# Kernel tuning notes

Hardware: AMD Instinct MI355X
Metric: run time of the kernel (lower is better)

## Reference

```python
import jax, jax.numpy as jnp
import numpy as np

N_NODES = 50000
N_EDGES = 400000
D_IN = 256
D_OUT = 256
DROPOUT_P = 0.1


def setup_inputs() -> dict:
    key = jax.random.key(0)
    k_feat, k_w, k_src, k_dst = jax.random.split(key, 4)
    feat = jax.random.normal(k_feat, (N_NODES, D_IN), dtype=jnp.float32)
    # Glorot-ish init for the GraphConv weight
    W = jax.random.normal(k_w, (D_IN, D_OUT), dtype=jnp.float32) * (1.0 / np.sqrt(D_IN))
    b = jnp.zeros((D_OUT,), dtype=jnp.float32)
    src = jax.random.randint(k_src, (N_EDGES,), 0, N_NODES, dtype=jnp.int32)
    dst = jax.random.randint(k_dst, (N_EDGES,), 0, N_NODES, dtype=jnp.int32)
    return {"feat": feat, "W": W, "b": b, "src": src, "dst": dst}


def reference(feat, W, b, src, dst):
    # Degrees from the edge list (DGL GraphConv norm='both'):
    # src is normalized by out-degree, dst by in-degree; clamp to >= 1.
    ones = jnp.ones((src.shape[0],), dtype=feat.dtype)
    deg_out = jnp.clip(jax.ops.segment_sum(ones, src, num_segments=N_NODES), 1.0)
    deg_in = jnp.clip(jax.ops.segment_sum(ones, dst, num_segments=N_NODES), 1.0)

    # Pre-normalize, project, then gather-scatter aggregate (mult W first,
    # mathematically identical to DGL's ordering since dims are equal).
    x = feat * jax.lax.rsqrt(deg_out)[:, None]          # [N, D_in]
    x = x @ W                                            # [N, D_out]
    agg = jax.ops.segment_sum(x[src], dst, num_segments=N_NODES)  # [N, D_out]
    h = agg * jax.lax.rsqrt(deg_in)[:, None] + b

    # Activation + dropout (training-mode, deterministic key)
    h = jax.nn.relu(h)
    keep = jax.random.bernoulli(jax.random.key(42), 1.0 - DROPOUT_P, h.shape)
    h = jnp.where(keep, h / (1.0 - DROPOUT_P), 0.0)
    return h
```

## Files before the change

### kernel.cpp

```cpp
#include <hip/hip_runtime.h>
#include <stdint.h>

#define N_NODES 50000
#define N_EDGES 400000
#define DDIM 256
#define MASK_WORDS 400000
#define EDGE_CAP 64
#define EDGE_BLOCKS 782
#define MASK_BLOCKS 1563
#define FCONV_BLOCKS 6250

typedef __attribute__((ext_vector_type(8))) short bf16x8;
typedef __attribute__((ext_vector_type(4))) float f32x4;

__device__ __forceinline__ uint32_t rotl32(uint32_t x, uint32_t r) {
  return (x << r) | (x >> (32u - r));
}

__device__ __forceinline__ uint32_t threefry_draw_0_42(uint32_t x0, uint32_t x1) {
  const uint32_t k0 = 0u, k1 = 42u;
  const uint32_t k2 = k0 ^ k1 ^ 0x1BD11BDAu;
  x0 += k0;
  x1 += k1;
#define TF_ROUND(r)          \
  {                          \
    x0 += x1;                \
    x1 = rotl32(x1, r);      \
    x1 ^= x0;                \
  }
  TF_ROUND(13) TF_ROUND(15) TF_ROUND(26) TF_ROUND(6)
  x0 += k1; x1 += k2 + 1u;
  TF_ROUND(17) TF_ROUND(29) TF_ROUND(16) TF_ROUND(24)
  x0 += k2; x1 += k0 + 2u;
  TF_ROUND(13) TF_ROUND(15) TF_ROUND(26) TF_ROUND(6)
  x0 += k0; x1 += k1 + 3u;
  TF_ROUND(17) TF_ROUND(29) TF_ROUND(16) TF_ROUND(24)
  x0 += k1; x1 += k2 + 4u;
  TF_ROUND(13) TF_ROUND(15) TF_ROUND(26) TF_ROUND(6)
  x0 += k2; x1 += k0 + 5u;
#undef TF_ROUND
  return x0 ^ x1;
}

__device__ __forceinline__ uint16_t bf16_rne(float x) {
  uint32_t u = __float_as_uint(x);
  u += 0x7FFFu + ((u >> 16) & 1u);
  return (uint16_t)(u >> 16);
}

__global__ __launch_bounds__(256) void setup_kernel(
    const float* __restrict__ W, uint16_t* __restrict__ Wt,
    int4* __restrict__ zero_base) {
  const int bid = blockIdx.x;
  if (bid < 98) {
    const int t = bid * 256 + threadIdx.x;
    if (t < 25000) zero_base[t] = make_int4(0, 0, 0, 0);
  } else {
    const int t = (bid - 98) * 256 + threadIdx.x;
    const int n = t >> 6;
    const int k4 = (t & 63) << 2;
    ushort4 p;
    p.x = bf16_rne(W[(size_t)(k4 + 0) * DDIM + n]);
    p.y = bf16_rne(W[(size_t)(k4 + 1) * DDIM + n]);
    p.z = bf16_rne(W[(size_t)(k4 + 2) * DDIM + n]);
    p.w = bf16_rne(W[(size_t)(k4 + 3) * DDIM + n]);
    *(ushort4*)(Wt + (size_t)n * DDIM + k4) = p;
  }
}

__global__ __launch_bounds__(256) void mega_prep_kernel(
    const float* __restrict__ feat, const int* __restrict__ src,
    const int* __restrict__ dst, int* __restrict__ deg_out,
    int* __restrict__ deg_in, int* __restrict__ esrc,
    uint32_t* __restrict__ mask, uint16_t* __restrict__ featb) {
  const int bid = blockIdx.x;
  if (bid < EDGE_BLOCKS) {
    const int base = (bid * 256 + threadIdx.x) * 2;
    if (base < N_EDGES) {
      const int2 s2 = *(const int2*)(src + base);
      const int2 d2 = *(const int2*)(dst + base);
      atomicAdd(&deg_out[s2.x], 1);
      atomicAdd(&deg_out[s2.y], 1);
      const int p0 = atomicAdd(&deg_in[d2.x], 1);
      const int p1 = atomicAdd(&deg_in[d2.y], 1);
      if (p0 < EDGE_CAP) esrc[(d2.x << 6) + p0] = s2.x;
      if (p1 < EDGE_CAP) esrc[(d2.y << 6) + p1] = s2.y;
    }
  } else if (bid < EDGE_BLOCKS + MASK_BLOCKS) {
    const uint32_t t =
        (uint32_t)(bid - EDGE_BLOCKS) * 256u + (uint32_t)threadIdx.x;
    if (t < MASK_WORDS) {
      const uint32_t base = t * 32u;
      uint32_t w = 0u;
#pragma unroll
      for (uint32_t b = 0; b < 32u; ++b) {
        const uint32_t bits = threefry_draw_0_42(0u, base + b);
        w |= ((bits >> 9) < 7549747u) ? (1u << b) : 0u;
      }
      mask[t] = w;
    }
  } else {
    const int t = (bid - EDGE_BLOCKS - MASK_BLOCKS) * 256 + threadIdx.x;
    const size_t base = (size_t)t * 8;
    const float4 a = *(const float4*)(feat + base);
    const float4 b = *(const float4*)(feat + base + 4);
    ushort4 lo, hi;
    lo.x = bf16_rne(a.x); lo.y = bf16_rne(a.y);
    lo.z = bf16_rne(a.z); lo.w = bf16_rne(a.w);
    hi.x = bf16_rne(b.x); hi.y = bf16_rne(b.y);
    hi.z = bf16_rne(b.z); hi.w = bf16_rne(b.w);
    *(ushort4*)(featb + base) = lo;
    *(ushort4*)(featb + base + 4) = hi;
  }
}

__device__ __forceinline__ void acc4s(float* a, uint2 q, float sc) {
  a[0] = fmaf(__uint_as_float(q.x << 16), sc, a[0]);
  a[1] = fmaf(__uint_as_float(q.x & 0xFFFF0000u), sc, a[1]);
  a[2] = fmaf(__uint_as_float(q.y << 16), sc, a[2]);
  a[3] = fmaf(__uint_as_float(q.y & 0xFFFF0000u), sc, a[3]);
}

__device__ __forceinline__ float dscale(const int* deg, int s) {
  return rsqrtf(fmaxf((float)deg[s], 1.0f));
}

__global__ __launch_bounds__(256) void gather_kernel(
    const uint16_t* __restrict__ featb, const int* __restrict__ deg_out,
    const int* __restrict__ deg_in, const int* __restrict__ esrc,
    uint16_t* __restrict__ agg) {
  const int n = blockIdx.x * 4 + (threadIdx.x >> 6);
  if (n >= N_NODES) return;
  const int lane = threadIdx.x & 63;
  const size_t coff = (size_t)(lane << 2);
  const int beg = n << 6;
  const int cnt = min(deg_in[n], EDGE_CAP);

  float a[4] = {};
  int j = 0;
  for (; j + 8 <= cnt; j += 8) {
    const int4 e0 = *(const int4*)(esrc + beg + j);
    const int4 e1 = *(const int4*)(esrc + beg + j + 4);
    const uint2 q0 = *(const uint2*)(featb + (size_t)e0.x * DDIM + coff);
    const uint2 q1 = *(const uint2*)(featb + (size_t)e0.y * DDIM + coff);
    const uint2 q2 = *(const uint2*)(featb + (size_t)e0.z * DDIM + coff);
    const uint2 q3 = *(const uint2*)(featb + (size_t)e0.w * DDIM + coff);
    const uint2 q4 = *(const uint2*)(featb + (size_t)e1.x * DDIM + coff);
    const uint2 q5 = *(const uint2*)(featb + (size_t)e1.y * DDIM + coff);
    const uint2 q6 = *(const uint2*)(featb + (size_t)e1.z * DDIM + coff);
    const uint2 q7 = *(const uint2*)(featb + (size_t)e1.w * DDIM + coff);
    const float s0 = dscale(deg_out, e0.x);
    const float s1 = dscale(deg_out, e0.y);
    const float s2 = dscale(deg_out, e0.z);
    const float s3 = dscale(deg_out, e0.w);
    const float s4 = dscale(deg_out, e1.x);
    const float s5 = dscale(deg_out, e1.y);
    const float s6 = dscale(deg_out, e1.z);
    const float s7 = dscale(deg_out, e1.w);
    acc4s(a, q0, s0); acc4s(a, q1, s1); acc4s(a, q2, s2); acc4s(a, q3, s3);
    acc4s(a, q4, s4); acc4s(a, q5, s5); acc4s(a, q6, s6); acc4s(a, q7, s7);
  }
  if (j + 4 <= cnt) {
    const int4 e0 = *(const int4*)(esrc + beg + j);
    const uint2 q0 = *(const uint2*)(featb + (size_t)e0.x * DDIM + coff);
    const uint2 q1 = *(const uint2*)(featb + (size_t)e0.y * DDIM + coff);
    const uint2 q2 = *(const uint2*)(featb + (size_t)e0.z * DDIM + coff);
    const uint2 q3 = *(const uint2*)(featb + (size_t)e0.w * DDIM + coff);
    const float s0 = dscale(deg_out, e0.x);
    const float s1 = dscale(deg_out, e0.y);
    const float s2 = dscale(deg_out, e0.z);
    const float s3 = dscale(deg_out, e0.w);
    acc4s(a, q0, s0); acc4s(a, q1, s1); acc4s(a, q2, s2); acc4s(a, q3, s3);
    j += 4;
  }
  if (j + 2 <= cnt) {
    const int s0i = esrc[beg + j];
    const int s1i = esrc[beg + j + 1];
    const uint2 q0 = *(const uint2*)(featb + (size_t)s0i * DDIM + coff);
    const uint2 q1 = *(const uint2*)(featb + (size_t)s1i * DDIM + coff);
    acc4s(a, q0, dscale(deg_out, s0i));
    acc4s(a, q1, dscale(deg_out, s1i));
    j += 2;
  }
  if (j < cnt) {
    const int s0i = esrc[beg + j];
    const uint2 q0 = *(const uint2*)(featb + (size_t)s0i * DDIM + coff);
    acc4s(a, q0, dscale(deg_out, s0i));
  }

  uint2 p;
  p.x = (uint32_t)bf16_rne(a[0]) | ((uint32_t)bf16_rne(a[1]) << 16);
  p.y = (uint32_t)bf16_rne(a[2]) | ((uint32_t)bf16_rne(a[3]) << 16);
  *(uint2*)(agg + (size_t)n * DDIM + coff) = p;
}

#define APAD 280
__global__ __launch_bounds__(256, 4) void gemm_mfma_kernel(
    const uint16_t* __restrict__ agg, const uint16_t* __restrict__ Wt,
    const float* __restrict__ bias, const int* __restrict__ deg_in,
    const uint32_t* __restrict__ mask, float* __restrict__ out) {
  __shared__ short As[64 * APAD];
  __shared__ float sdeg[64];
  __shared__ float sbias[256];

  const int tid = threadIdx.x;
  const int r0 = blockIdx.x * 64;
  const int lane = tid & 63;
  const int seg = lane >> 4;
  const int l15 = lane & 15;
  const int wc = tid >> 6;

  sbias[tid] = bias[tid];
  if (tid < 64) {
    const int r = r0 + tid;
    sdeg[tid] = (r < N_NODES) ? rsqrtf(fmaxf((float)deg_in[r], 1.0f)) : 0.0f;
  }

  {
    const uint16_t* ap = agg + (size_t)r0 * DDIM;
#pragma unroll
    for (int it = 0; it < 8; ++it) {
      const int c = tid + 256 * it;
      const int row = c >> 5;
      const int k8 = (c & 31) << 3;
      int4 v = make_int4(0, 0, 0, 0);
      if (r0 + row < N_NODES) v = *(const int4*)(ap + (size_t)row * DDIM + k8);
      *(int4*)&As[row * APAD + k8] = v;
    }
  }
  __syncthreads();

  const uint16_t* wt_base = Wt + (size_t)(wc * 64 + l15) * DDIM + seg * 8;

  f32x4 acc[4][4] = {};
#pragma unroll
  for (int kkI = 0; kkI < 8; ++kkI) {
    const int kk = kkI * 32;
    bf16x8 a[4], b[4];
#pragma unroll
    for (int m = 0; m < 4; ++m)
      a[m] = *(const bf16x8*)&As[(m * 16 + l15) * APAD + kk + seg * 8];
#pragma unroll
    for (int n = 0; n < 4; ++n)
      b[n] = *(const bf16x8*)(wt_base + n * 16 * DDIM + kk);
#pragma unroll
    for (int m = 0; m < 4; ++m)
#pragma unroll
      for (int n = 0; n < 4; ++n)
        acc[m][n] = __builtin_amdgcn_mfma_f32_16x16x32_bf16(a[m], b[n], acc[m][n], 0, 0, 0);
  }

  constexpr float INV09 = 1.0f / 0.9f;
#pragma unroll
  for (int m = 0; m < 4; ++m) {
#pragma unroll
    for (int r = 0; r < 4; ++r) {
      const int lrow = m * 16 + seg * 4 + r;
      const int row = r0 + lrow;
      if (row >= N_NODES) continue;
      const float s = sdeg[lrow];
      const uint32_t w0 = mask[row * 8 + wc * 2];
      const uint32_t w1 = mask[row * 8 + wc * 2 + 1];
#pragma unroll
      for (int n = 0; n < 4; ++n) {
        const int col = wc * 64 + n * 16 + l15;
        float v = fmaxf(acc[m][n][r] * s + sbias[col], 0.0f);
        const uint32_t w = (n < 2) ? w0 : w1;
        const uint32_t bit = (uint32_t)((n & 1) * 16 + l15);
        out[(size_t)row * DDIM + col] = ((w >> bit) & 1u) ? v * INV09 : 0.0f;
      }
    }
  }
}

extern "C" void kernel_launch(void* const* d_in, const int* in_sizes, int n_in,
                              void* d_out, int out_size, void* d_ws, size_t ws_size,
                              hipStream_t stream) {
  const float* feat = (const float*)d_in[0];
  const float* W = (const float*)d_in[1];
  const float* bias = (const float*)d_in[2];
  const int* src = (const int*)d_in[3];
  const int* dst = (const int*)d_in[4];
  float* out = (float*)d_out;

  char* ws = (char*)d_ws;
  int* deg_out = (int*)(ws + 0);
  int* deg_in = (int*)(ws + 200000);
  int* esrc = (int*)(ws + 400000);
  uint16_t* Wt = (uint16_t*)(ws + 13200000);
  uint16_t* featb = (uint16_t*)(ws + 13331072);
  uint32_t* mask = (uint32_t*)(ws + 38931072);
  uint16_t* agg = (uint16_t*)(ws + 40531072);

  setup_kernel<<<162, 256, 0, stream>>>(W, Wt, (int4*)d_ws);
  mega_prep_kernel<<<EDGE_BLOCKS + MASK_BLOCKS + FCONV_BLOCKS, 256, 0, stream>>>(
      feat, src, dst, deg_out, deg_in, esrc, mask, featb);
  gather_kernel<<<(N_NODES + 3) / 4, 256, 0, stream>>>(featb, deg_out, deg_in, esrc, agg);
  gemm_mfma_kernel<<<(N_NODES + 63) / 64, 256, 0, stream>>>(agg, Wt, bias, deg_in, mask, out);
}
```

Before: 129.8 us.

## Move dropout mask generation into gather kernel and widen edge-degree threads

The compute-heavy threefry dropout-mask generation moves out of the prep kernel and is interleaved as every ninth block of the memory-bound gather kernel, so ALU work can overlap the gather's scattered loads. The edge-degree phase now handles eight edges per thread with int4 loads, using a quarter as many blocks. The interleaved grid adds index arithmetic and makes gather block scheduling less regular, and each edge thread now has a longer chain of atomics.

```diff
diff --git a/kernel.cpp b/kernel.cpp
--- a/kernel.cpp
+++ b/kernel.cpp
@@ -6,8 +6,7 @@
 #define DDIM 256
 #define MASK_WORDS 400000
 #define EDGE_CAP 64
-#define EDGE_BLOCKS 782
-#define MASK_BLOCKS 1563
+#define EDGE_BLOCKS 196
 #define FCONV_BLOCKS 6250
 
 typedef __attribute__((ext_vector_type(8))) short bf16x8;
@@ -72,35 +71,42 @@
     const float* __restrict__ feat, const int* __restrict__ src,
     const int* __restrict__ dst, int* __restrict__ deg_out,
     int* __restrict__ deg_in, int* __restrict__ esrc,
-    uint32_t* __restrict__ mask, uint16_t* __restrict__ featb) {
+    uint16_t* __restrict__ featb) {
   const int bid = blockIdx.x;
   if (bid < EDGE_BLOCKS) {
-    const int base = (bid * 256 + threadIdx.x) * 2;
+    const int base = (bid * 256 + threadIdx.x) * 8;
     if (base < N_EDGES) {
-      const int2 s2 = *(const int2*)(src + base);
-      const int2 d2 = *(const int2*)(dst + base);
-      atomicAdd(&deg_out[s2.x], 1);
-      atomicAdd(&deg_out[s2.y], 1);
-      const int p0 = atomicAdd(&deg_in[d2.x], 1);
-      const int p1 = atomicAdd(&deg_in[d2.y], 1);
-      if (p0 < EDGE_CAP) esrc[(d2.x << 6) + p0] = s2.x;
-      if (p1 < EDGE_CAP) esrc[(d2.y << 6) + p1] = s2.y;
-    }
-  } else if (bid < EDGE_BLOCKS + MASK_BLOCKS) {
-    const uint32_t t =
-        (uint32_t)(bid - EDGE_BLOCKS) * 256u + (uint32_t)threadIdx.x;
-    if (t < MASK_WORDS) {
-      const uint32_t base = t * 32u;
-      uint32_t w = 0u;
-#pragma unroll
-      for (uint32_t b = 0; b < 32u; ++b) {
-        const uint32_t bits = threefry_draw_0_42(0u, base + b);
-        w |= ((bits >> 9) < 7549747u) ? (1u << b) : 0u;
-      }
-      mask[t] = w;
+      const int4 sa = *(const int4*)(src + base);
+      const int4 sb = *(const int4*)(src + base + 4);
+      const int4 da = *(const int4*)(dst + base);
+      const int4 db = *(const int4*)(dst + base + 4);
+      atomicAdd(&deg_out[sa.x], 1);
+      atomicAdd(&deg_out[sa.y], 1);
+      atomicAdd(&deg_out[sa.z], 1);
+      atomicAdd(&deg_out[sa.w], 1);
+      atomicAdd(&deg_out[sb.x], 1);
+      atomicAdd(&deg_out[sb.y], 1);
+      atomicAdd(&deg_out[sb.z], 1);
+      atomicAdd(&deg_out[sb.w], 1);
+      const int p0 = atomicAdd(&deg_in[da.x], 1);
+      const int p1 = atomicAdd(&deg_in[da.y], 1);
+      const int p2 = atomicAdd(&deg_in[da.z], 1);
+      const int p3 = atomicAdd(&deg_in[da.w], 1);
+      const int p4 = atomicAdd(&deg_in[db.x], 1);
+      const int p5 = atomicAdd(&deg_in[db.y], 1);
+      const int p6 = atomicAdd(&deg_in[db.z], 1);
+      const int p7 = atomicAdd(&deg_in[db.w], 1);
+      if (p0 < EDGE_CAP) esrc[(da.x << 6) + p0] = sa.x;
+      if (p1 < EDGE_CAP) esrc[(da.y << 6) + p1] = sa.y;
+      if (p2 < EDGE_CAP) esrc[(da.z << 6) + p2] = sa.z;
+      if (p3 < EDGE_CAP) esrc[(da.w << 6) + p3] = sa.w;
+      if (p4 < EDGE_CAP) esrc[(db.x << 6) + p4] = sb.x;
+      if (p5 < EDGE_CAP) esrc[(db.y << 6) + p5] = sb.y;
+      if (p6 < EDGE_CAP) esrc[(db.z << 6) + p6] = sb.z;
+      if (p7 < EDGE_CAP) esrc[(db.w << 6) + p7] = sb.w;
     }
   } else {
-    const int t = (bid - EDGE_BLOCKS - MASK_BLOCKS) * 256 + threadIdx.x;
+    const int t = (bid - EDGE_BLOCKS) * 256 + threadIdx.x;
     const size_t base = (size_t)t * 8;
     const float4 a = *(const float4*)(feat + base);
     const float4 b = *(const float4*)(feat + base + 4);
@@ -125,13 +131,32 @@
   return rsqrtf(fmaxf((float)deg[s], 1.0f));
 }
 
-__global__ __launch_bounds__(256) void gather_kernel(
+__global__ __launch_bounds__(256) void gather_mask_kernel(
     const uint16_t* __restrict__ featb, const int* __restrict__ deg_out,
     const int* __restrict__ deg_in, const int* __restrict__ esrc,
-    uint16_t* __restrict__ agg) {
-  const int n = blockIdx.x * 4 + (threadIdx.x >> 6);
+    uint16_t* __restrict__ agg, uint32_t* __restrict__ mask) {
+  const int bid = blockIdx.x;
+  const int tid = threadIdx.x;
+
+  if ((bid % 9) == 8) {
+    const uint32_t t = (uint32_t)(bid / 9) * 256u + (uint32_t)tid;
+    if (t < MASK_WORDS) {
+      const uint32_t base = t * 32u;
+      uint32_t w = 0u;
+#pragma unroll
+      for (uint32_t b = 0; b < 32u; ++b) {
+        const uint32_t bits = threefry_draw_0_42(0u, base + b);
+        w |= ((bits >> 9) < 7549747u) ? (1u << b) : 0u;
+      }
+      mask[t] = w;
+    }
+    return;
+  }
+
+  const int g = (bid / 9) * 8 + (bid % 9);
+  const int n = g * 4 + (tid >> 6);
   if (n >= N_NODES) return;
-  const int lane = threadIdx.x & 63;
+  const int lane = tid & 63;
   const size_t coff = (size_t)(lane << 2);
   const int beg = n << 6;
   const int cnt = min(deg_in[n], EDGE_CAP);
@@ -293,8 +318,8 @@
   uint16_t* agg = (uint16_t*)(ws + 40531072);
 
   setup_kernel<<<162, 256, 0, stream>>>(W, Wt, (int4*)d_ws);
-  mega_prep_kernel<<<EDGE_BLOCKS + MASK_BLOCKS + FCONV_BLOCKS, 256, 0, stream>>>(
-      feat, src, dst, deg_out, deg_in, esrc, mask, featb);
-  gather_kernel<<<(N_NODES + 3) / 4, 256, 0, stream>>>(featb, deg_out, deg_in, esrc, agg);
+  mega_prep_kernel<<<EDGE_BLOCKS + FCONV_BLOCKS, 256, 0, stream>>>(
+      feat, src, dst, deg_out, deg_in, esrc, featb);
+  gather_mask_kernel<<<14067, 256, 0, stream>>>(featb, deg_out, deg_in, esrc, agg, mask);
   gemm_mfma_kernel<<<(N_NODES + 63) / 64, 256, 0, stream>>>(agg, Wt, bias, deg_in, mask, out);
 }
```

Result: no change. 130.9 us (+0.9%).
